# Kernel tuning notes

Hardware: AMD Instinct MI355X
Metric: run time of the kernel (lower is better)

The kernel has to match this reference:

```python
import jax, jax.numpy as jnp
import numpy as np

C, T, H = 256, 16, 8
D = C // H  # head dim = 32
SCALE = float((D * T) ** 0.5)


def setup_inputs() -> dict:
    key = jax.random.key(0)
    kx, kk, kq, kv = jax.random.split(key, 4)
    B, P = 8, 1024
    x = jax.random.normal(kx, (B, C, P, T), dtype=jnp.float32)
    # 1x1 conv weights, no bias -> [out_ch, in_ch]
    Wk = jax.random.normal(kk, (C, C), dtype=jnp.float32) * 0.02
    Wq = jax.random.normal(kq, (C, C), dtype=jnp.float32) * 0.02
    Wv = jax.random.normal(kv, (C, C), dtype=jnp.float32) * 0.02
    return {"x": x, "Wk": Wk, "Wq": Wq, "Wv": Wv}


def _proj_split(W, x):
    # 1x1 conv == channel matmul, then split heads: b (h d) p t -> b h d p t
    B, _, P, Tt = x.shape
    y = jnp.einsum('oc,bcpt->bopt', W, x)
    return y.reshape(B, H, D, P, Tt)


def reference(x, Wk, Wq, Wv):
    B, _, P, Tt = x.shape
    k = _proj_split(Wk, x)  # [B,H,D,P,T]
    q = _proj_split(Wq, x)
    v = _proj_split(Wv, x)
    # energy over spatial positions, contracting head-dim and time
    energy = jnp.einsum('bhdpt,bhdqt->bhpq', k, q)  # [B,H,P,P]
    attn = jax.nn.softmax(energy / SCALE, axis=-1)
    out = jnp.einsum('bhpq,bhdpt->bhdqt', attn, v)  # [B,H,D,P,T]
    return out.reshape(B, C, P, Tt)
```

## Files before the change

kernel.cpp:

```cpp
#include <hip/hip_runtime.h>


typedef unsigned short u16;
typedef unsigned int u32;
typedef __attribute__((ext_vector_type(8))) short bfx8;
typedef __attribute__((ext_vector_type(4))) float fx4;

constexpr float KC1 = 1.4426950408889634f / 22.627416997969522f;

__device__ __forceinline__ u16 f2bf(float f) {
  u32 u = __builtin_bit_cast(u32, f);
  return (u16)((u + 0x7fffu + ((u >> 16) & 1u)) >> 16);
}
__device__ __forceinline__ float bf2f(u16 v) {
  return __builtin_bit_cast(float, (u32)v << 16);
}
__device__ __forceinline__ fx4 mfma16(bfx8 a, bfx8 b, fx4 c) {
  return __builtin_amdgcn_mfma_f32_16x16x32_bf16(a, b, c, 0, 0, 0);
}
typedef __attribute__((address_space(1))) const unsigned int* as1p;
typedef __attribute__((address_space(3))) unsigned int* as3p;
__device__ __forceinline__ void gll16(const void* g, void* l) {
  __builtin_amdgcn_global_load_lds((as1p)g, (as3p)l, 16, 0, 0);
}

template <int NT, int LK>
__device__ __forceinline__ void gemm_core(const u16* __restrict__ Ag,
                                          const u16* __restrict__ Bg,
                                          u16 (&As)[3][16384], u16 (&Bs)[2][16384],
                                          fx4 (&acc)[8][4], int wv, int lane) {
  const int l15 = lane & 15, kg = lane >> 4, l7 = lane & 7;
  const int wq0 = (wv >> 2) * 128, wn0 = (wv & 3) * 64;
  const int rsub = lane >> 3, csub = (lane & 7) * 8;

  auto stageA = [&](int buf, int ks) {
#pragma unroll
    for (int i = 0; i < 4; ++i) {
      int r = wv * 32 + i * 8;
      gll16(Ag + (size_t)(r + rsub) * LK + ks * 64 + csub, &As[buf][r * 64]);
    }
  };
  auto stageB = [&](int buf, int ks) {
#pragma unroll
    for (int i = 0; i < 4; ++i) {
      int r = wv * 32 + i * 8;
      gll16(Bg + (size_t)(r + rsub) * LK + ks * 64 + csub, &Bs[buf][r * 64]);
    }
  };
  auto comp = [&](int ab, int bb) {
#pragma unroll
    for (int kk = 0; kk < 2; ++kk) {
      int csw = ((kk * 4 + kg) ^ l7) * 8;
      bfx8 af[8];
#pragma unroll
      for (int mt = 0; mt < 8; ++mt)
        af[mt] = *(const bfx8*)&As[ab][(wq0 + mt * 16 + l15) * 64 + csw];
#pragma unroll
      for (int nt = 0; nt < 4; ++nt) {
        bfx8 bf = *(const bfx8*)&Bs[bb][(wn0 + nt * 16 + l15) * 64 + csw];
#pragma unroll
        for (int mt = 0; mt < 8; ++mt) acc[mt][nt] = mfma16(af[mt], bf, acc[mt][nt]);
      }
    }
  };

  stageA(0, 0);
  stageB(0, 0);
  stageA(1, 1);
  stageB(1, 1);
  asm volatile("s_waitcnt vmcnt(8)" ::: "memory");
  __builtin_amdgcn_s_barrier();
  __builtin_amdgcn_sched_barrier(0);

  int ca = 0;
#pragma unroll 1
  for (int t = 0; t < NT; ++t) {
    const int cb = t & 1;
    if (t + 2 < NT) {
      int ca2 = ca + 2; if (ca2 >= 3) ca2 -= 3;
      stageA(ca2, t + 2);
    }
    __builtin_amdgcn_s_setprio(1);
    comp(ca, cb);
    __builtin_amdgcn_s_setprio(0);
    if (t + 1 < NT) {
      if (t + 2 < NT) {
        asm volatile("s_waitcnt vmcnt(4)" ::: "memory");
      } else {
        asm volatile("s_waitcnt vmcnt(0)" ::: "memory");
      }
      __builtin_amdgcn_s_barrier();
      __builtin_amdgcn_sched_barrier(0);
      if (t + 2 < NT) stageB(cb, t + 2);
    }
    ca = (ca == 2) ? 0 : ca + 1;
  }
}

__global__ __launch_bounds__(256) void k_wconv(const float* __restrict__ Wk,
                                               const float* __restrict__ Wq,
                                               const float* __restrict__ Wv,
                                               u16* __restrict__ Wall) {
  int blk = blockIdx.x;
  int pr = blk >> 5;
  const float* src = (pr == 0) ? Wk : ((pr == 1) ? Wq : Wv);
  int oc = (blk & 31) * 8 + (threadIdx.x >> 5);
  int Cc = threadIdx.x & 31;
  const float4* s4 = (const float4*)(src + oc * 256 + Cc * 8);
  float4 a = s4[0], b = s4[1];
  alignas(16) u16 t[8] = {f2bf(a.x), f2bf(a.y), f2bf(a.z), f2bf(a.w),
                          f2bf(b.x), f2bf(b.y), f2bf(b.z), f2bf(b.w)};
  int o = pr * 256 + oc;
  int pos = (Cc & ~7) + ((Cc & 7) ^ (o & 7));
  *(uint4*)(Wall + o * 256 + pos * 8) = *(const uint4*)t;
}

__global__ __launch_bounds__(256) void k_xt(const float* __restrict__ x,
                                            u16* __restrict__ Xbf) {
  __shared__ u16 Xs[128 * 256];
  int b = blockIdx.x >> 7;
  int n0 = (blockIdx.x & 127) * 128;
  int tid = threadIdx.x;
  int ng = tid & 31, cgrp = tid >> 5;
  const float* xb = x + (size_t)b * 4194304 + n0 + ng * 4;
#pragma unroll
  for (int it = 0; it < 4; ++it) {
    int Cc = cgrp + it * 8;
    float4 v[8];
#pragma unroll
    for (int i = 0; i < 8; ++i)
      v[i] = *(const float4*)(xb + (size_t)(Cc * 8 + i) * 16384);
#pragma unroll
    for (int j = 0; j < 4; ++j) {
      int n = ng * 4 + j;
      alignas(16) u16 c8[8];
#pragma unroll
      for (int i = 0; i < 8; ++i) c8[i] = f2bf(((const float*)&v[i])[j]);
      int pos = (Cc & ~7) + ((Cc & 7) ^ (n & 7));
      *(uint4*)&Xs[n * 256 + pos * 8] = *(const uint4*)c8;
    }
  }
  __syncthreads();
  u16* xo = Xbf + (size_t)b * 4194304 + (size_t)n0 * 256;
#pragma unroll
  for (int it = 0; it < 16; ++it) {
    int idx = tid + it * 256;
    int n = idx >> 5, chp = idx & 31;
    uint4 v = *(const uint4*)&Xs[n * 256 + chp * 8];
    *(uint4*)&xo[(size_t)n * 256 + chp * 8] = v;
  }
}

__global__ __launch_bounds__(512) void k_proj2(const u16* __restrict__ Xbf,
                                               const u16* __restrict__ Wall,
                                               u16* __restrict__ Kb, u16* __restrict__ Qb,
                                               u16* __restrict__ Vb) {
  __shared__ u16 As[3][16384];
  __shared__ u16 Bs[2][16384];
  int bid = blockIdx.x;
  int vid = (bid & 7) * 192 + (bid >> 3);
  int nidx = vid / 3;
  int otile = vid - nidx * 3;
  int b = nidx >> 6, ntile = nidx & 63;
  int tid = threadIdx.x, lane = tid & 63, wv = tid >> 6;
  int l15 = lane & 15, kg = lane >> 4;
  int wq0 = (wv >> 2) * 128;
  const u16* Ag = Wall + otile * 65536;
  const u16* Bg = Xbf + (size_t)b * 4194304 + (size_t)ntile * 65536;
  fx4 acc[8][4];
#pragma unroll
  for (int mt = 0; mt < 8; ++mt)
#pragma unroll
    for (int nt = 0; nt < 4; ++nt) acc[mt][nt] = (fx4)0.0f;

  gemm_core<4, 256>(Ag, Bg, As, Bs, acc, wv, lane);

  u16* dst = (otile == 0) ? Kb : ((otile == 1) ? Qb : Vb);
#pragma unroll
  for (int mt = 0; mt < 8; ++mt) {
    int oc = wq0 + mt * 16 + kg * 4;
    int h = oc >> 5;
    size_t bhro = (size_t)(b * 8 + h) * 524288;
#pragma unroll
    for (int nt = 0; nt < 4; ++nt) {
      int p = ntile * 16 + (wv & 3) * 4 + nt;
      size_t ro = bhro + (size_t)p * 512;
      int p7 = p & 7;
#pragma unroll
      for (int j = 0; j < 4; ++j) {
        int f = ((oc & 31) + j) * 16 + l15;
        int ch = (f >> 3) ^ p7;
        dst[ro + ch * 8 + (f & 7)] = f2bf(acc[mt][nt][j]);
      }
    }
  }
}

__global__ __launch_bounds__(512) void k_egemm(const u16* __restrict__ Qb,
                                               const u16* __restrict__ Kb,
                                               u16* __restrict__ Pt,
                                               float* __restrict__ Zpart) {
  __shared__ u16 As[3][16384];
  __shared__ u16 Bs[2][16384];
  int bid = blockIdx.x;
  int vid = (bid & 7) * 128 + (bid >> 3);
  int bh = vid >> 4, tile = vid & 15;
  int q0 = (tile >> 2) * 256, p0 = (tile & 3) * 256;
  int tid = threadIdx.x, lane = tid & 63, wv = tid >> 6;
  int l15 = lane & 15, kg = lane >> 4;
  int wq0 = (wv >> 2) * 128, wp0 = (wv & 3) * 64;
  const u16* Ag = Qb + (size_t)bh * 524288 + (size_t)q0 * 512;
  const u16* Bg = Kb + (size_t)bh * 524288 + (size_t)p0 * 512;
  fx4 acc[8][4];
#pragma unroll
  for (int mt = 0; mt < 8; ++mt)
#pragma unroll
    for (int nt = 0; nt < 4; ++nt) acc[mt][nt] = (fx4)0.0f;

  gemm_core<8, 512>(Ag, Bg, As, Bs, acc, wv, lane);

  float zl[4] = {0.f, 0.f, 0.f, 0.f};
  size_t pbase = (size_t)bh * 1048576;
#pragma unroll
  for (int mt = 0; mt < 8; ++mt) {
    int qb_ = q0 + wq0 + mt * 16 + kg * 4;
#pragma unroll
    for (int nt = 0; nt < 4; ++nt) {
      int p = p0 + wp0 + nt * 16 + l15;
#pragma unroll
      for (int j = 0; j < 4; ++j) {
        int q = qb_ + j;
        float e = exp2f(acc[mt][nt][j] * KC1);
        zl[nt] += e;
        Pt[pbase + (size_t)q * 1024 + (((p >> 3) ^ (q & 7)) * 8 + (p & 7))] = f2bf(e);
      }
    }
  }
  float* Zl = (float*)&As[0][0];
#pragma unroll
  for (int nt = 0; nt < 4; ++nt) {
    float v = zl[nt];
    v += __shfl_xor(v, 16);
    v += __shfl_xor(v, 32);
    zl[nt] = v;
  }
  if (lane < 16) {
#pragma unroll
    for (int nt = 0; nt < 4; ++nt)
      Zl[(wv >> 2) * 256 + wp0 + nt * 16 + lane] = zl[nt];
  }
  __syncthreads();
  if (tid < 256) {
    float s = Zl[tid] + Zl[256 + tid];
    Zpart[(size_t)(tile >> 2) * 65536 + (size_t)bh * 1024 + p0 + tid] = s;
  }
}

__global__ __launch_bounds__(256) void k_zfinal(const float* __restrict__ Zpart,
                                                float* __restrict__ RZ) {
  int idx = blockIdx.x * 256 + threadIdx.x;
  float s = Zpart[idx] + Zpart[65536 + idx] + Zpart[131072 + idx] + Zpart[196608 + idx];
  RZ[idx] = 1.0f / s;
}

__global__ __launch_bounds__(256) void k_vt(const u16* __restrict__ Vb,
                                            const float* __restrict__ RZ,
                                            u16* __restrict__ Vt) {
  __shared__ u16 Vl[64 * 512];
  int bh = blockIdx.x >> 4;
  int ptile = blockIdx.x & 15;
  int tid = threadIdx.x;
  const u16* src = Vb + (size_t)bh * 524288 + (size_t)ptile * 32768;
#pragma unroll
  for (int it = 0; it < 16; ++it) {
    int idx = tid + it * 256;
    int pl = idx >> 6, g = idx & 63;
    float rz = RZ[bh * 1024 + ptile * 64 + pl];
    uint4 v = *(const uint4*)&src[(size_t)pl * 512 + g * 8];
    int cf = g ^ (pl & 7);
    u32 w[4] = {v.x, v.y, v.z, v.w};
    alignas(16) u16 c8[8];
#pragma unroll
    for (int i = 0; i < 4; ++i) {
      c8[2 * i]     = f2bf(bf2f((u16)w[i]) * rz);
      c8[2 * i + 1] = f2bf(bf2f((u16)(w[i] >> 16)) * rz);
    }
    *(uint4*)&Vl[pl * 512 + cf * 8] = *(const uint4*)c8;
  }
  __syncthreads();
  u16* dst = Vt + (size_t)bh * 524288;
#pragma unroll
  for (int it = 0; it < 16; ++it) {
    int f = (tid & 63) + (it & 7) * 64;
    int pc = (tid >> 6) * 2 + (it >> 3);
    int base = pc * 8 * 512 + f;
    u32 x0 = (u32)Vl[base] | ((u32)Vl[base + 512] << 16);
    u32 x1 = (u32)Vl[base + 1024] | ((u32)Vl[base + 1536] << 16);
    u32 x2 = (u32)Vl[base + 2048] | ((u32)Vl[base + 2560] << 16);
    u32 x3 = (u32)Vl[base + 3072] | ((u32)Vl[base + 3584] << 16);
    uint4 pk; pk.x = x0; pk.y = x1; pk.z = x2; pk.w = x3;
    int col = ptile * 8 + (pc ^ (f & 7));
    *(uint4*)&dst[(size_t)f * 1024 + col * 8] = pk;
  }
}

__global__ __launch_bounds__(512) void k_pv(const u16* __restrict__ Pt,
                                            const u16* __restrict__ Vt,
                                            float* __restrict__ out) {
  __shared__ u16 As[3][16384];
  __shared__ u16 Bs[2][16384];
  int bid = blockIdx.x;
  int vid = (bid & 7) * 64 + (bid >> 3);
  int bh = vid >> 3, tile = vid & 7;
  int q0 = (tile >> 1) * 256, f0 = (tile & 1) * 256;
  int tid = threadIdx.x, lane = tid & 63, wv = tid >> 6;
  int l15 = lane & 15, kg = lane >> 4;
  int wq0 = (wv >> 2) * 128, wf0 = (wv & 3) * 64;
  const u16* Ag = Pt + (size_t)bh * 1048576 + (size_t)q0 * 1024;
  const u16* Bg = Vt + (size_t)bh * 524288 + (size_t)f0 * 1024;
  fx4 acc[8][4];
#pragma unroll
  for (int mt = 0; mt < 8; ++mt)
#pragma unroll
    for (int nt = 0; nt < 4; ++nt) acc[mt][nt] = (fx4)0.0f;

  gemm_core<16, 1024>(Ag, Bg, As, Bs, acc, wv, lane);

#pragma unroll
  for (int mt = 0; mt < 8; ++mt) {
    int qb_ = q0 + wq0 + mt * 16 + kg * 4;
#pragma unroll
    for (int nt = 0; nt < 4; ++nt) {
      int f = f0 + wf0 + nt * 16 + l15;
      int d = f >> 4, t = f & 15;
      size_t cb = (size_t)(bh * 32 + d) * 16384 + t;
#pragma unroll
      for (int j = 0; j < 4; ++j) out[cb + (size_t)(qb_ + j) * 16] = acc[mt][nt][j];
    }
  }
}

extern "C" void kernel_launch(void* const* d_in, const int* in_sizes, int n_in,
                              void* d_out, int out_size, void* d_ws, size_t ws_size,
                              hipStream_t stream) {
  (void)in_sizes; (void)n_in; (void)out_size; (void)ws_size;
  const float* x  = (const float*)d_in[0];
  const float* Wk = (const float*)d_in[1];
  const float* Wq = (const float*)d_in[2];
  const float* Wv = (const float*)d_in[3];
  float* out = (float*)d_out;

  u16* Kb  = (u16*)d_ws;
  u16* Qb  = Kb + 33554432;
  u16* Vb  = Qb + 33554432;
  u16* Xbf = Vb + 33554432;
  u16* Pt  = Xbf;
  u16* Vt  = Qb;
  float* Zpart = (float*)(Kb + 167772160);
  float* RZ = Zpart + 262144;
  u16* Wall = (u16*)(RZ + 65536);

  k_wconv<<<96, 256, 0, stream>>>(Wk, Wq, Wv, Wall);
  k_xt<<<1024, 256, 0, stream>>>(x, Xbf);
  k_proj2<<<1536, 512, 0, stream>>>(Xbf, Wall, Kb, Qb, Vb);
  k_egemm<<<1024, 512, 0, stream>>>(Qb, Kb, Pt, Zpart);
  k_zfinal<<<256, 256, 0, stream>>>(Zpart, RZ);
  k_vt<<<1024, 256, 0, stream>>>(Vb, RZ, Vt);
  k_pv<<<512, 512, 0, stream>>>(Pt, Vt, out);
}
```

Measured before the change: 389.0 us.

## Replace GEMM core with 8-phase ping-pong pipeline over half-tiles

Replaces the triple/double-buffered GEMM main loop shared by the projection, energy and PV kernels with an 8-phase schedule. It splits each 256x256 tile into M/N halves, double-buffers A and B in one LDS array, and interleaves half-tile global->LDS loads with register fragment loads and MFMA bursts between barriers. The warp-to-output mapping changes to 2x4 sub-blocks spread across halves, and the epilogues are adjusted to match. The aim is to overlap memory traffic with MFMA work at finer grain, at the cost of many more barriers per K step and tighter waitcnt bookkeeping.

```diff
diff --git a/kernel.cpp b/kernel.cpp
--- a/kernel.cpp
+++ b/kernel.cpp
@@ -23,77 +23,113 @@
 __device__ __forceinline__ void gll16(const void* g, void* l) {
   __builtin_amdgcn_global_load_lds((as1p)g, (as3p)l, 16, 0, 0);
 }
-
-template <int NT, int LK>
-__device__ __forceinline__ void gemm_core(const u16* __restrict__ Ag,
-                                          const u16* __restrict__ Bg,
-                                          u16 (&As)[3][16384], u16 (&Bs)[2][16384],
-                                          fx4 (&acc)[8][4], int wv, int lane) {
-  const int l15 = lane & 15, kg = lane >> 4, l7 = lane & 7;
-  const int wq0 = (wv >> 2) * 128, wn0 = (wv & 3) * 64;
-  const int rsub = lane >> 3, csub = (lane & 7) * 8;
-
-  auto stageA = [&](int buf, int ks) {
-#pragma unroll
-    for (int i = 0; i < 4; ++i) {
-      int r = wv * 32 + i * 8;
-      gll16(Ag + (size_t)(r + rsub) * LK + ks * 64 + csub, &As[buf][r * 64]);
-    }
-  };
-  auto stageB = [&](int buf, int ks) {
-#pragma unroll
-    for (int i = 0; i < 4; ++i) {
-      int r = wv * 32 + i * 8;
-      gll16(Bg + (size_t)(r + rsub) * LK + ks * 64 + csub, &Bs[buf][r * 64]);
-    }
-  };
-  auto comp = [&](int ab, int bb) {
-#pragma unroll
-    for (int kk = 0; kk < 2; ++kk) {
-      int csw = ((kk * 4 + kg) ^ l7) * 8;
-      bfx8 af[8];
-#pragma unroll
-      for (int mt = 0; mt < 8; ++mt)
-        af[mt] = *(const bfx8*)&As[ab][(wq0 + mt * 16 + l15) * 64 + csw];
-#pragma unroll
-      for (int nt = 0; nt < 4; ++nt) {
-        bfx8 bf = *(const bfx8*)&Bs[bb][(wn0 + nt * 16 + l15) * 64 + csw];
-#pragma unroll
-        for (int mt = 0; mt < 8; ++mt) acc[mt][nt] = mfma16(af[mt], bf, acc[mt][nt]);
-      }
-    }
-  };
-
-  stageA(0, 0);
-  stageB(0, 0);
-  stageA(1, 1);
-  stageB(1, 1);
-  asm volatile("s_waitcnt vmcnt(8)" ::: "memory");
+__device__ __forceinline__ void bar_() {
   __builtin_amdgcn_s_barrier();
   __builtin_amdgcn_sched_barrier(0);
-
-  int ca = 0;
+}
+__device__ __forceinline__ void lg0_() {
+  asm volatile("s_waitcnt lgkmcnt(0)" ::: "memory");
+  __builtin_amdgcn_sched_barrier(0);
+}
+#define VMC4 asm volatile("s_waitcnt vmcnt(4)" ::: "memory")
+#define VMC0 asm volatile("s_waitcnt vmcnt(0)" ::: "memory")
+
+template <int NT, int LK>
+__device__ __forceinline__ void gemm8(const u16* __restrict__ Ag,
+                                      const u16* __restrict__ Bg,
+                                      u16* lds, fx4 (&acc)[2][4][2][2],
+                                      int wv, int lane) {
+  const int l15 = lane & 15, kg = lane >> 4, l7 = lane & 7;
+  const int wr = wv >> 2, wn = wv & 3;
+  const int rsub = lane >> 3, csub = (lane & 7) * 8;
+  constexpr int A0 = 0, A1 = 16384, B0 = 32768, B1 = 49152;
+  bfx8 af[4][2], bf[2][2][2];
+
+  auto stg = [&](const u16* g, int ldsoff, int tile, int half) {
+    const u16* gp = g + (size_t)(half * 128 + wv * 16 + rsub) * LK + tile * 64 + csub;
+    u16* lp = lds + ldsoff + half * 8192 + wv * 1024;
+    gll16(gp, lp);
+    gll16(gp + (size_t)8 * LK, lp + 512);
+  };
+  auto LA = [&](int boff, int mh) {
+    const u16* base = lds + boff + mh * 8192 + wr * 4096;
+#pragma unroll
+    for (int mt = 0; mt < 4; ++mt)
+#pragma unroll
+      for (int kk = 0; kk < 2; ++kk)
+        af[mt][kk] = *(const bfx8*)(base + (mt * 16 + l15) * 64 + (((kk << 2) + kg) ^ l7) * 8);
+  };
+  auto LB = [&](int boff, int nh) {
+    const u16* base = lds + boff + nh * 8192 + wn * 2048;
+#pragma unroll
+    for (int nt = 0; nt < 2; ++nt)
+#pragma unroll
+      for (int kk = 0; kk < 2; ++kk)
+        bf[nh][nt][kk] = *(const bfx8*)(base + (nt * 16 + l15) * 64 + (((kk << 2) + kg) ^ l7) * 8);
+  };
+  auto MM = [&](int mh, int nh) {
+    __builtin_amdgcn_s_setprio(1);
+#pragma unroll
+    for (int mt = 0; mt < 4; ++mt)
+#pragma unroll
+      for (int nt = 0; nt < 2; ++nt)
+#pragma unroll
+        for (int kk = 0; kk < 2; ++kk)
+          acc[mh][mt][nh][nt] = mfma16(af[mt][kk], bf[nh][nt][kk], acc[mh][mt][nh][nt]);
+    __builtin_amdgcn_s_setprio(0);
+  };
+
+  stg(Ag, A0, 0, 0); stg(Ag, A0, 0, 1);
+  stg(Bg, B0, 0, 0); stg(Bg, B0, 0, 1);
+  stg(Ag, A1, 1, 0); stg(Bg, B1, 1, 1);
+  VMC4;
+  bar_();
+
+  constexpr int NI = NT / 2;
 #pragma unroll 1
-  for (int t = 0; t < NT; ++t) {
-    const int cb = t & 1;
-    if (t + 2 < NT) {
-      int ca2 = ca + 2; if (ca2 >= 3) ca2 -= 3;
-      stageA(ca2, t + 2);
-    }
-    __builtin_amdgcn_s_setprio(1);
-    comp(ca, cb);
-    __builtin_amdgcn_s_setprio(0);
-    if (t + 1 < NT) {
-      if (t + 2 < NT) {
-        asm volatile("s_waitcnt vmcnt(4)" ::: "memory");
-      } else {
-        asm volatile("s_waitcnt vmcnt(0)" ::: "memory");
-      }
-      __builtin_amdgcn_s_barrier();
-      __builtin_amdgcn_sched_barrier(0);
-      if (t + 2 < NT) stageB(cb, t + 2);
-    }
-    ca = (ca == 2) ? 0 : ca + 1;
+  for (int i = 0; i < NI; ++i) {
+    const int t = 2 * i;
+    const bool more = (i + 1 < NI);
+    LA(A0, 0); LB(B0, 0);
+    stg(Ag, A1, t + 1, 1);
+    bar_(); lg0_();
+    MM(0, 0);
+    bar_();
+    LB(B0, 1);
+    stg(Bg, B1, t + 1, 0);
+    bar_(); lg0_();
+    MM(0, 1);
+    bar_();
+    LA(A0, 1);
+    if (more) stg(Ag, A0, t + 2, 0);
+    bar_(); lg0_();
+    MM(1, 1);
+    bar_();
+    if (more) stg(Bg, B0, t + 2, 1);
+    bar_();
+    MM(1, 0);
+    if (more) { VMC4; } else { VMC0; }
+    bar_();
+    LA(A1, 0); LB(B1, 0);
+    if (more) stg(Ag, A0, t + 2, 1);
+    bar_(); lg0_();
+    MM(0, 0);
+    bar_();
+    LB(B1, 1);
+    if (more) stg(Bg, B0, t + 2, 0);
+    bar_(); lg0_();
+    MM(0, 1);
+    bar_();
+    LA(A1, 1);
+    if (more) stg(Ag, A1, t + 3, 0);
+    bar_(); lg0_();
+    MM(1, 1);
+    bar_();
+    if (more) stg(Bg, B1, t + 3, 1);
+    bar_();
+    MM(1, 0);
+    if (more) { VMC4; }
+    bar_();
   }
 }
 
@@ -155,8 +191,7 @@
                                                const u16* __restrict__ Wall,
                                                u16* __restrict__ Kb, u16* __restrict__ Qb,
                                                u16* __restrict__ Vb) {
-  __shared__ u16 As[3][16384];
-  __shared__ u16 Bs[2][16384];
+  __shared__ u16 lds[65536];
   int bid = blockIdx.x;
   int vid = (bid & 7) * 192 + (bid >> 3);
   int nidx = vid / 3;
@@ -164,90 +199,110 @@
   int b = nidx >> 6, ntile = nidx & 63;
   int tid = threadIdx.x, lane = tid & 63, wv = tid >> 6;
   int l15 = lane & 15, kg = lane >> 4;
-  int wq0 = (wv >> 2) * 128;
+  int wr = wv >> 2, wn = wv & 3;
   const u16* Ag = Wall + otile * 65536;
   const u16* Bg = Xbf + (size_t)b * 4194304 + (size_t)ntile * 65536;
-  fx4 acc[8][4];
-#pragma unroll
-  for (int mt = 0; mt < 8; ++mt)
-#pragma unroll
-    for (int nt = 0; nt < 4; ++nt) acc[mt][nt] = (fx4)0.0f;
-
-  gemm_core<4, 256>(Ag, Bg, As, Bs, acc, wv, lane);
+  fx4 acc[2][4][2][2];
+#pragma unroll
+  for (int mh = 0; mh < 2; ++mh)
+#pragma unroll
+    for (int mt = 0; mt < 4; ++mt)
+#pragma unroll
+      for (int nh = 0; nh < 2; ++nh)
+#pragma unroll
+        for (int nt = 0; nt < 2; ++nt) acc[mh][mt][nh][nt] = (fx4)0.0f;
+
+  gemm8<4, 256>(Ag, Bg, lds, acc, wv, lane);
 
   u16* dst = (otile == 0) ? Kb : ((otile == 1) ? Qb : Vb);
 #pragma unroll
-  for (int mt = 0; mt < 8; ++mt) {
-    int oc = wq0 + mt * 16 + kg * 4;
-    int h = oc >> 5;
-    size_t bhro = (size_t)(b * 8 + h) * 524288;
-#pragma unroll
-    for (int nt = 0; nt < 4; ++nt) {
-      int p = ntile * 16 + (wv & 3) * 4 + nt;
-      size_t ro = bhro + (size_t)p * 512;
-      int p7 = p & 7;
-#pragma unroll
-      for (int j = 0; j < 4; ++j) {
-        int f = ((oc & 31) + j) * 16 + l15;
-        int ch = (f >> 3) ^ p7;
-        dst[ro + ch * 8 + (f & 7)] = f2bf(acc[mt][nt][j]);
-      }
-    }
-  }
+  for (int mh = 0; mh < 2; ++mh)
+#pragma unroll
+    for (int mt = 0; mt < 4; ++mt) {
+      int o = mh * 128 + wr * 64 + mt * 16 + kg * 4;
+      int h = o >> 5;
+      size_t bhro = (size_t)(b * 8 + h) * 524288;
+#pragma unroll
+      for (int nh = 0; nh < 2; ++nh)
+#pragma unroll
+        for (int nt = 0; nt < 2; ++nt) {
+          int p = ntile * 16 + nh * 8 + wn * 2 + nt;
+          size_t ro = bhro + (size_t)p * 512;
+          int p7 = p & 7;
+#pragma unroll
+          for (int j = 0; j < 4; ++j) {
+            int f = ((o & 31) + j) * 16 + l15;
+            int ch = (f >> 3) ^ p7;
+            dst[ro + ch * 8 + (f & 7)] = f2bf(acc[mh][mt][nh][nt][j]);
+          }
+        }
+    }
 }
 
 __global__ __launch_bounds__(512) void k_egemm(const u16* __restrict__ Qb,
                                                const u16* __restrict__ Kb,
                                                u16* __restrict__ Pt,
                                                float* __restrict__ Zpart) {
-  __shared__ u16 As[3][16384];
-  __shared__ u16 Bs[2][16384];
+  __shared__ u16 lds[65536];
   int bid = blockIdx.x;
   int vid = (bid & 7) * 128 + (bid >> 3);
   int bh = vid >> 4, tile = vid & 15;
   int q0 = (tile >> 2) * 256, p0 = (tile & 3) * 256;
   int tid = threadIdx.x, lane = tid & 63, wv = tid >> 6;
   int l15 = lane & 15, kg = lane >> 4;
-  int wq0 = (wv >> 2) * 128, wp0 = (wv & 3) * 64;
+  int wr = wv >> 2, wn = wv & 3;
   const u16* Ag = Qb + (size_t)bh * 524288 + (size_t)q0 * 512;
   const u16* Bg = Kb + (size_t)bh * 524288 + (size_t)p0 * 512;
-  fx4 acc[8][4];
-#pragma unroll
-  for (int mt = 0; mt < 8; ++mt)
-#pragma unroll
-    for (int nt = 0; nt < 4; ++nt) acc[mt][nt] = (fx4)0.0f;
-
-  gemm_core<8, 512>(Ag, Bg, As, Bs, acc, wv, lane);
-
-  float zl[4] = {0.f, 0.f, 0.f, 0.f};
+  fx4 acc[2][4][2][2];
+#pragma unroll
+  for (int mh = 0; mh < 2; ++mh)
+#pragma unroll
+    for (int mt = 0; mt < 4; ++mt)
+#pragma unroll
+      for (int nh = 0; nh < 2; ++nh)
+#pragma unroll
+        for (int nt = 0; nt < 2; ++nt) acc[mh][mt][nh][nt] = (fx4)0.0f;
+
+  gemm8<8, 512>(Ag, Bg, lds, acc, wv, lane);
+
+  float zl[2][2] = {{0.f, 0.f}, {0.f, 0.f}};
   size_t pbase = (size_t)bh * 1048576;
 #pragma unroll
-  for (int mt = 0; mt < 8; ++mt) {
-    int qb_ = q0 + wq0 + mt * 16 + kg * 4;
-#pragma unroll
-    for (int nt = 0; nt < 4; ++nt) {
-      int p = p0 + wp0 + nt * 16 + l15;
-#pragma unroll
-      for (int j = 0; j < 4; ++j) {
-        int q = qb_ + j;
-        float e = exp2f(acc[mt][nt][j] * KC1);
-        zl[nt] += e;
-        Pt[pbase + (size_t)q * 1024 + (((p >> 3) ^ (q & 7)) * 8 + (p & 7))] = f2bf(e);
-      }
-    }
-  }
-  float* Zl = (float*)&As[0][0];
-#pragma unroll
-  for (int nt = 0; nt < 4; ++nt) {
-    float v = zl[nt];
-    v += __shfl_xor(v, 16);
-    v += __shfl_xor(v, 32);
-    zl[nt] = v;
-  }
+  for (int mh = 0; mh < 2; ++mh)
+#pragma unroll
+    for (int mt = 0; mt < 4; ++mt) {
+      int qb_ = q0 + mh * 128 + wr * 64 + mt * 16 + kg * 4;
+#pragma unroll
+      for (int nh = 0; nh < 2; ++nh)
+#pragma unroll
+        for (int nt = 0; nt < 2; ++nt) {
+          int p = p0 + nh * 128 + wn * 32 + nt * 16 + l15;
+#pragma unroll
+          for (int j = 0; j < 4; ++j) {
+            int q = qb_ + j;
+            float e = exp2f(acc[mh][mt][nh][nt][j] * KC1);
+            zl[nh][nt] += e;
+            Pt[pbase + (size_t)q * 1024 + (((p >> 3) ^ (q & 7)) * 8 + (p & 7))] = f2bf(e);
+          }
+        }
+    }
+  float* Zl = (float*)lds;
+#pragma unroll
+  for (int nh = 0; nh < 2; ++nh)
+#pragma unroll
+    for (int nt = 0; nt < 2; ++nt) {
+      float v = zl[nh][nt];
+      v += __shfl_xor(v, 16);
+      v += __shfl_xor(v, 32);
+      zl[nh][nt] = v;
+    }
+  __syncthreads();
   if (lane < 16) {
 #pragma unroll
-    for (int nt = 0; nt < 4; ++nt)
-      Zl[(wv >> 2) * 256 + wp0 + nt * 16 + lane] = zl[nt];
+    for (int nh = 0; nh < 2; ++nh)
+#pragma unroll
+      for (int nt = 0; nt < 2; ++nt)
+        Zl[wr * 256 + nh * 128 + wn * 32 + nt * 16 + lane] = zl[nh][nt];
   }
   __syncthreads();
   if (tid < 256) {
@@ -307,37 +362,44 @@
 __global__ __launch_bounds__(512) void k_pv(const u16* __restrict__ Pt,
                                             const u16* __restrict__ Vt,
                                             float* __restrict__ out) {
-  __shared__ u16 As[3][16384];
-  __shared__ u16 Bs[2][16384];
+  __shared__ u16 lds[65536];
   int bid = blockIdx.x;
   int vid = (bid & 7) * 64 + (bid >> 3);
   int bh = vid >> 3, tile = vid & 7;
   int q0 = (tile >> 1) * 256, f0 = (tile & 1) * 256;
   int tid = threadIdx.x, lane = tid & 63, wv = tid >> 6;
   int l15 = lane & 15, kg = lane >> 4;
-  int wq0 = (wv >> 2) * 128, wf0 = (wv & 3) * 64;
+  int wr = wv >> 2, wn = wv & 3;
   const u16* Ag = Pt + (size_t)bh * 1048576 + (size_t)q0 * 1024;
   const u16* Bg = Vt + (size_t)bh * 524288 + (size_t)f0 * 1024;
-  fx4 acc[8][4];
-#pragma unroll
-  for (int mt = 0; mt < 8; ++mt)
-#pragma unroll
-    for (int nt = 0; nt < 4; ++nt) acc[mt][nt] = (fx4)0.0f;
-
-  gemm_core<16, 1024>(Ag, Bg, As, Bs, acc, wv, lane);
-
-#pragma unroll
-  for (int mt = 0; mt < 8; ++mt) {
-    int qb_ = q0 + wq0 + mt * 16 + kg * 4;
-#pragma unroll
-    for (int nt = 0; nt < 4; ++nt) {
-      int f = f0 + wf0 + nt * 16 + l15;
-      int d = f >> 4, t = f & 15;
-      size_t cb = (size_t)(bh * 32 + d) * 16384 + t;
-#pragma unroll
-      for (int j = 0; j < 4; ++j) out[cb + (size_t)(qb_ + j) * 16] = acc[mt][nt][j];
-    }
-  }
+  fx4 acc[2][4][2][2];
+#pragma unroll
+  for (int mh = 0; mh < 2; ++mh)
+#pragma unroll
+    for (int mt = 0; mt < 4; ++mt)
+#pragma unroll
+      for (int nh = 0; nh < 2; ++nh)
+#pragma unroll
+        for (int nt = 0; nt < 2; ++nt) acc[mh][mt][nh][nt] = (fx4)0.0f;
+
+  gemm8<16, 1024>(Ag, Bg, lds, acc, wv, lane);
+
+#pragma unroll
+  for (int mh = 0; mh < 2; ++mh)
+#pragma unroll
+    for (int mt = 0; mt < 4; ++mt) {
+      int qb_ = q0 + mh * 128 + wr * 64 + mt * 16 + kg * 4;
+#pragma unroll
+      for (int nh = 0; nh < 2; ++nh)
+#pragma unroll
+        for (int nt = 0; nt < 2; ++nt) {
+          int f = f0 + nh * 128 + wn * 32 + nt * 16 + l15;
+          int d = f >> 4, t = f & 15;
+          size_t cb = (size_t)(bh * 32 + d) * 16384 + t;
+#pragma unroll
+          for (int j = 0; j < 4; ++j) out[cb + (size_t)(qb_ + j) * 16] = acc[mh][mt][nh][nt][j];
+        }
+    }
 }
 
 extern "C" void kernel_launch(void* const* d_in, const int* in_sizes, int n_in,
```

Measured after the change: 352.7 us. 9.3% less time.

## Replace pipelined 256x256 GEMM core with simple 128x128 single-buffer tiles

Applied to the files above, without the earlier changes.

Swaps the triple/double-buffered 256x256 GEMM core (512 threads, about 160KB of LDS) for a simpler 128x128 tile using 256 threads and 32KB of LDS with launch_bounds occupancy 3. This trades data reuse and explicit load/compute overlap for higher occupancy, so several blocks per CU can hide latency. The energy GEMM swaps its MFMA operands so each lane can write 4 contiguous bf16 P values as one 64-bit store, and the Z partial sums grow to 16 slices with shuffle reductions. Risks include more global/L2 traffic from smaller tiles and the loss of the software pipeline, since there is a sync before and after every load stage.

```diff
diff --git a/kernel.cpp b/kernel.cpp
--- a/kernel.cpp
+++ b/kernel.cpp
@@ -3,6 +3,7 @@
 
 typedef unsigned short u16;
 typedef unsigned int u32;
+typedef unsigned long long u64;
 typedef __attribute__((ext_vector_type(8))) short bfx8;
 typedef __attribute__((ext_vector_type(4))) float fx4;
 
@@ -24,76 +25,49 @@
   __builtin_amdgcn_global_load_lds((as1p)g, (as3p)l, 16, 0, 0);
 }
 
-template <int NT, int LK>
-__device__ __forceinline__ void gemm_core(const u16* __restrict__ Ag,
-                                          const u16* __restrict__ Bg,
-                                          u16 (&As)[3][16384], u16 (&Bs)[2][16384],
-                                          fx4 (&acc)[8][4], int wv, int lane) {
+template <bool SWAP, int NT, int LK>
+__device__ __forceinline__ void gemm97(const u16* __restrict__ Ag,
+                                       const u16* __restrict__ Bg,
+                                       u16* lds, fx4 (&acc)[4][4],
+                                       int wv, int lane) {
   const int l15 = lane & 15, kg = lane >> 4, l7 = lane & 7;
-  const int wq0 = (wv >> 2) * 128, wn0 = (wv & 3) * 64;
+  const int wr = wv >> 1, wc = wv & 1;
   const int rsub = lane >> 3, csub = (lane & 7) * 8;
-
-  auto stageA = [&](int buf, int ks) {
+  bfx8 af[4][2], bf[4][2];
+
+#pragma unroll 1
+  for (int t = 0; t < NT; ++t) {
+    __syncthreads();
 #pragma unroll
     for (int i = 0; i < 4; ++i) {
       int r = wv * 32 + i * 8;
-      gll16(Ag + (size_t)(r + rsub) * LK + ks * 64 + csub, &As[buf][r * 64]);
-    }
-  };
-  auto stageB = [&](int buf, int ks) {
-#pragma unroll
-    for (int i = 0; i < 4; ++i) {
-      int r = wv * 32 + i * 8;
-      gll16(Bg + (size_t)(r + rsub) * LK + ks * 64 + csub, &Bs[buf][r * 64]);
-    }
-  };
-  auto comp = [&](int ab, int bb) {
-#pragma unroll
-    for (int kk = 0; kk < 2; ++kk) {
-      int csw = ((kk * 4 + kg) ^ l7) * 8;
-      bfx8 af[8];
-#pragma unroll
-      for (int mt = 0; mt < 8; ++mt)
-        af[mt] = *(const bfx8*)&As[ab][(wq0 + mt * 16 + l15) * 64 + csw];
-#pragma unroll
-      for (int nt = 0; nt < 4; ++nt) {
-        bfx8 bf = *(const bfx8*)&Bs[bb][(wn0 + nt * 16 + l15) * 64 + csw];
-#pragma unroll
-        for (int mt = 0; mt < 8; ++mt) acc[mt][nt] = mfma16(af[mt], bf, acc[mt][nt]);
-      }
-    }
-  };
-
-  stageA(0, 0);
-  stageB(0, 0);
-  stageA(1, 1);
-  stageB(1, 1);
-  asm volatile("s_waitcnt vmcnt(8)" ::: "memory");
-  __builtin_amdgcn_s_barrier();
-  __builtin_amdgcn_sched_barrier(0);
-
-  int ca = 0;
-#pragma unroll 1
-  for (int t = 0; t < NT; ++t) {
-    const int cb = t & 1;
-    if (t + 2 < NT) {
-      int ca2 = ca + 2; if (ca2 >= 3) ca2 -= 3;
-      stageA(ca2, t + 2);
-    }
-    __builtin_amdgcn_s_setprio(1);
-    comp(ca, cb);
-    __builtin_amdgcn_s_setprio(0);
-    if (t + 1 < NT) {
-      if (t + 2 < NT) {
-        asm volatile("s_waitcnt vmcnt(4)" ::: "memory");
-      } else {
-        asm volatile("s_waitcnt vmcnt(0)" ::: "memory");
-      }
-      __builtin_amdgcn_s_barrier();
-      __builtin_amdgcn_sched_barrier(0);
-      if (t + 2 < NT) stageB(cb, t + 2);
-    }
-    ca = (ca == 2) ? 0 : ca + 1;
+      gll16(Ag + (size_t)(r + rsub) * LK + t * 64 + csub, lds + r * 64);
+      gll16(Bg + (size_t)(r + rsub) * LK + t * 64 + csub, lds + 8192 + r * 64);
+    }
+    __syncthreads();
+#pragma unroll
+    for (int mt = 0; mt < 4; ++mt)
+#pragma unroll
+      for (int kk = 0; kk < 2; ++kk)
+        af[mt][kk] = *(const bfx8*)(lds + (wr * 64 + mt * 16 + l15) * 64 +
+                                    (((kk << 2) + kg) ^ l7) * 8);
+#pragma unroll
+    for (int nt = 0; nt < 4; ++nt)
+#pragma unroll
+      for (int kk = 0; kk < 2; ++kk)
+        bf[nt][kk] = *(const bfx8*)(lds + 8192 + (wc * 64 + nt * 16 + l15) * 64 +
+                                    (((kk << 2) + kg) ^ l7) * 8);
+#pragma unroll
+    for (int mt = 0; mt < 4; ++mt)
+#pragma unroll
+      for (int nt = 0; nt < 4; ++nt)
+#pragma unroll
+        for (int kk = 0; kk < 2; ++kk) {
+          if constexpr (SWAP)
+            acc[mt][nt] = mfma16(bf[nt][kk], af[mt][kk], acc[mt][nt]);
+          else
+            acc[mt][nt] = mfma16(af[mt][kk], bf[nt][kk], acc[mt][nt]);
+        }
   }
 }
 
@@ -133,11 +107,11 @@
 #pragma unroll
     for (int j = 0; j < 4; ++j) {
       int n = ng * 4 + j;
-      alignas(16) u16 c8[8];
-#pragma unroll
-      for (int i = 0; i < 8; ++i) c8[i] = f2bf(((const float*)&v[i])[j]);
+      alignas(16) u16 c8v[8];
+#pragma unroll
+      for (int i = 0; i < 8; ++i) c8v[i] = f2bf(((const float*)&v[i])[j]);
       int pos = (Cc & ~7) + ((Cc & 7) ^ (n & 7));
-      *(uint4*)&Xs[n * 256 + pos * 8] = *(const uint4*)c8;
+      *(uint4*)&Xs[n * 256 + pos * 8] = *(const uint4*)c8v;
     }
   }
   __syncthreads();
@@ -151,44 +125,46 @@
   }
 }
 
-__global__ __launch_bounds__(512) void k_proj2(const u16* __restrict__ Xbf,
-                                               const u16* __restrict__ Wall,
-                                               u16* __restrict__ Kb, u16* __restrict__ Qb,
-                                               u16* __restrict__ Vb) {
-  __shared__ u16 As[3][16384];
-  __shared__ u16 Bs[2][16384];
+__global__ __launch_bounds__(256, 3) void k_proj2(const u16* __restrict__ Xbf,
+                                                  const u16* __restrict__ Wall,
+                                                  u16* __restrict__ Kb, u16* __restrict__ Qb,
+                                                  u16* __restrict__ Vb) {
+  __shared__ u16 lds[16384];
   int bid = blockIdx.x;
-  int vid = (bid & 7) * 192 + (bid >> 3);
-  int nidx = vid / 3;
-  int otile = vid - nidx * 3;
-  int b = nidx >> 6, ntile = nidx & 63;
+  int vid = (bid & 7) * 768 + (bid >> 3);
+  int b = vid / 768;
+  int rem = vid - b * 768;
+  int mtile = rem >> 7, ntile = rem & 127;
   int tid = threadIdx.x, lane = tid & 63, wv = tid >> 6;
   int l15 = lane & 15, kg = lane >> 4;
-  int wq0 = (wv >> 2) * 128;
-  const u16* Ag = Wall + otile * 65536;
-  const u16* Bg = Xbf + (size_t)b * 4194304 + (size_t)ntile * 65536;
-  fx4 acc[8][4];
-#pragma unroll
-  for (int mt = 0; mt < 8; ++mt)
+  int wr = wv >> 1, wc = wv & 1;
+  const u16* Ag = Wall + mtile * 32768;
+  const u16* Bg = Xbf + (size_t)b * 4194304 + (size_t)ntile * 32768;
+  fx4 acc[4][4];
+#pragma unroll
+  for (int mt = 0; mt < 4; ++mt)
 #pragma unroll
     for (int nt = 0; nt < 4; ++nt) acc[mt][nt] = (fx4)0.0f;
 
-  gemm_core<4, 256>(Ag, Bg, As, Bs, acc, wv, lane);
-
-  u16* dst = (otile == 0) ? Kb : ((otile == 1) ? Qb : Vb);
-#pragma unroll
-  for (int mt = 0; mt < 8; ++mt) {
-    int oc = wq0 + mt * 16 + kg * 4;
+  gemm97<false, 4, 256>(Ag, Bg, lds, acc, wv, lane);
+
+  int pr = mtile >> 1;
+  u16* dst = (pr == 0) ? Kb : ((pr == 1) ? Qb : Vb);
+  int obase = (mtile & 1) * 128 + wr * 64;
+#pragma unroll
+  for (int mt = 0; mt < 4; ++mt) {
+    int oc = obase + mt * 16 + kg * 4;
     int h = oc >> 5;
     size_t bhro = (size_t)(b * 8 + h) * 524288;
 #pragma unroll
     for (int nt = 0; nt < 4; ++nt) {
-      int p = ntile * 16 + (wv & 3) * 4 + nt;
+      int n = ntile * 128 + wc * 64 + nt * 16 + l15;
+      int p = n >> 4, tt = n & 15;
       size_t ro = bhro + (size_t)p * 512;
       int p7 = p & 7;
 #pragma unroll
       for (int j = 0; j < 4; ++j) {
-        int f = ((oc & 31) + j) * 16 + l15;
+        int f = ((oc & 31) + j) * 16 + tt;
         int ch = (f >> 3) ^ p7;
         dst[ro + ch * 8 + (f & 7)] = f2bf(acc[mt][nt][j]);
       }
@@ -196,70 +172,85 @@
   }
 }
 
-__global__ __launch_bounds__(512) void k_egemm(const u16* __restrict__ Qb,
-                                               const u16* __restrict__ Kb,
-                                               u16* __restrict__ Pt,
-                                               float* __restrict__ Zpart) {
-  __shared__ u16 As[3][16384];
-  __shared__ u16 Bs[2][16384];
+__global__ __launch_bounds__(256, 3) void k_egemm(const u16* __restrict__ Qb,
+                                                  const u16* __restrict__ Kb,
+                                                  u16* __restrict__ Pt,
+                                                  float* __restrict__ Zpart) {
+  __shared__ u16 lds[16384];
   int bid = blockIdx.x;
-  int vid = (bid & 7) * 128 + (bid >> 3);
-  int bh = vid >> 4, tile = vid & 15;
-  int q0 = (tile >> 2) * 256, p0 = (tile & 3) * 256;
+  int vid = (bid & 7) * 512 + (bid >> 3);
+  int bh = vid >> 6;
+  int rem = vid & 63;
+  int qt = rem >> 3, pt = rem & 7;
+  int q0 = qt * 128, p0 = pt * 128;
   int tid = threadIdx.x, lane = tid & 63, wv = tid >> 6;
   int l15 = lane & 15, kg = lane >> 4;
-  int wq0 = (wv >> 2) * 128, wp0 = (wv & 3) * 64;
+  int wr = wv >> 1, wc = wv & 1;
   const u16* Ag = Qb + (size_t)bh * 524288 + (size_t)q0 * 512;
   const u16* Bg = Kb + (size_t)bh * 524288 + (size_t)p0 * 512;
-  fx4 acc[8][4];
-#pragma unroll
-  for (int mt = 0; mt < 8; ++mt)
+  fx4 acc[4][4];
+#pragma unroll
+  for (int mt = 0; mt < 4; ++mt)
 #pragma unroll
     for (int nt = 0; nt < 4; ++nt) acc[mt][nt] = (fx4)0.0f;
 
-  gemm_core<8, 512>(Ag, Bg, As, Bs, acc, wv, lane);
-
-  float zl[4] = {0.f, 0.f, 0.f, 0.f};
+  gemm97<true, 8, 512>(Ag, Bg, lds, acc, wv, lane);
+
   size_t pbase = (size_t)bh * 1048576;
-#pragma unroll
-  for (int mt = 0; mt < 8; ++mt) {
-    int qb_ = q0 + wq0 + mt * 16 + kg * 4;
+  float zac[4][4];
+#pragma unroll
+  for (int nt = 0; nt < 4; ++nt)
+#pragma unroll
+    for (int j = 0; j < 4; ++j) zac[nt][j] = 0.f;
+#pragma unroll
+  for (int mt = 0; mt < 4; ++mt) {
+    int q = q0 + wr * 64 + mt * 16 + l15;
+    size_t qrow = pbase + (size_t)q * 1024;
+    int q7 = l15 & 7;
 #pragma unroll
     for (int nt = 0; nt < 4; ++nt) {
-      int p = p0 + wp0 + nt * 16 + l15;
+      int p4 = p0 + wc * 64 + nt * 16 + kg * 4;
+      alignas(8) u16 e4[4];
 #pragma unroll
       for (int j = 0; j < 4; ++j) {
-        int q = qb_ + j;
         float e = exp2f(acc[mt][nt][j] * KC1);
-        zl[nt] += e;
-        Pt[pbase + (size_t)q * 1024 + (((p >> 3) ^ (q & 7)) * 8 + (p & 7))] = f2bf(e);
+        zac[nt][j] += e;
+        e4[j] = f2bf(e);
       }
-    }
-  }
-  float* Zl = (float*)&As[0][0];
-#pragma unroll
-  for (int nt = 0; nt < 4; ++nt) {
-    float v = zl[nt];
-    v += __shfl_xor(v, 16);
-    v += __shfl_xor(v, 32);
-    zl[nt] = v;
-  }
-  if (lane < 16) {
-#pragma unroll
-    for (int nt = 0; nt < 4; ++nt)
-      Zl[(wv >> 2) * 256 + wp0 + nt * 16 + lane] = zl[nt];
-  }
-  __syncthreads();
-  if (tid < 256) {
-    float s = Zl[tid] + Zl[256 + tid];
-    Zpart[(size_t)(tile >> 2) * 65536 + (size_t)bh * 1024 + p0 + tid] = s;
+      int ch = (p4 >> 3) ^ q7;
+      *(u64*)(Pt + qrow + ch * 8 + (p4 & 7)) = *(const u64*)e4;
+    }
+  }
+#pragma unroll
+  for (int nt = 0; nt < 4; ++nt)
+#pragma unroll
+    for (int j = 0; j < 4; ++j) {
+      float v = zac[nt][j];
+      v += __shfl_xor(v, 1);
+      v += __shfl_xor(v, 2);
+      v += __shfl_xor(v, 4);
+      v += __shfl_xor(v, 8);
+      zac[nt][j] = v;
+    }
+  if (l15 == 0) {
+    size_t zb = (size_t)(qt * 2 + wr) * 65536 + (size_t)bh * 1024;
+#pragma unroll
+    for (int nt = 0; nt < 4; ++nt) {
+      int p4 = p0 + wc * 64 + nt * 16 + kg * 4;
+      float4 zv;
+      zv.x = zac[nt][0]; zv.y = zac[nt][1];
+      zv.z = zac[nt][2]; zv.w = zac[nt][3];
+      *(float4*)&Zpart[zb + p4] = zv;
+    }
   }
 }
 
 __global__ __launch_bounds__(256) void k_zfinal(const float* __restrict__ Zpart,
                                                 float* __restrict__ RZ) {
   int idx = blockIdx.x * 256 + threadIdx.x;
-  float s = Zpart[idx] + Zpart[65536 + idx] + Zpart[131072 + idx] + Zpart[196608 + idx];
+  float s = 0.f;
+#pragma unroll
+  for (int k = 0; k < 16; ++k) s += Zpart[(size_t)k * 65536 + idx];
   RZ[idx] = 1.0f / s;
 }
 
@@ -279,13 +270,13 @@
     uint4 v = *(const uint4*)&src[(size_t)pl * 512 + g * 8];
     int cf = g ^ (pl & 7);
     u32 w[4] = {v.x, v.y, v.z, v.w};
-    alignas(16) u16 c8[8];
+    alignas(16) u16 c8v[8];
 #pragma unroll
     for (int i = 0; i < 4; ++i) {
-      c8[2 * i]     = f2bf(bf2f((u16)w[i]) * rz);
-      c8[2 * i + 1] = f2bf(bf2f((u16)(w[i] >> 16)) * rz);
-    }
-    *(uint4*)&Vl[pl * 512 + cf * 8] = *(const uint4*)c8;
+      c8v[2 * i]     = f2bf(bf2f((u16)w[i]) * rz);
+      c8v[2 * i + 1] = f2bf(bf2f((u16)(w[i] >> 16)) * rz);
+    }
+    *(uint4*)&Vl[pl * 512 + cf * 8] = *(const uint4*)c8v;
   }
   __syncthreads();
   u16* dst = Vt + (size_t)bh * 524288;
@@ -304,38 +295,40 @@
   }
 }
 
-__global__ __launch_bounds__(512) void k_pv(const u16* __restrict__ Pt,
-                                            const u16* __restrict__ Vt,
-                                            float* __restrict__ out) {
-  __shared__ u16 As[3][16384];
-  __shared__ u16 Bs[2][16384];
+__global__ __launch_bounds__(256, 3) void k_pv(const u16* __restrict__ Pt,
+                                               const u16* __restrict__ Vt,
+                                               float* __restrict__ out) {
+  __shared__ u16 lds[16384];
   int bid = blockIdx.x;
-  int vid = (bid & 7) * 64 + (bid >> 3);
-  int bh = vid >> 3, tile = vid & 7;
-  int q0 = (tile >> 1) * 256, f0 = (tile & 1) * 256;
+  int vid = (bid & 7) * 256 + (bid >> 3);
+  int bh = vid >> 5;
+  int rem = vid & 31;
+  int qt = rem >> 2, ft = rem & 3;
+  int q0 = qt * 128, f0 = ft * 128;
   int tid = threadIdx.x, lane = tid & 63, wv = tid >> 6;
   int l15 = lane & 15, kg = lane >> 4;
-  int wq0 = (wv >> 2) * 128, wf0 = (wv & 3) * 64;
+  int wr = wv >> 1, wc = wv & 1;
   const u16* Ag = Pt + (size_t)bh * 1048576 + (size_t)q0 * 1024;
   const u16* Bg = Vt + (size_t)bh * 524288 + (size_t)f0 * 1024;
-  fx4 acc[8][4];
-#pragma unroll
-  for (int mt = 0; mt < 8; ++mt)
+  fx4 acc[4][4];
+#pragma unroll
+  for (int mt = 0; mt < 4; ++mt)
 #pragma unroll
     for (int nt = 0; nt < 4; ++nt) acc[mt][nt] = (fx4)0.0f;
 
-  gemm_core<16, 1024>(Ag, Bg, As, Bs, acc, wv, lane);
-
-#pragma unroll
-  for (int mt = 0; mt < 8; ++mt) {
-    int qb_ = q0 + wq0 + mt * 16 + kg * 4;
+  gemm97<false, 16, 1024>(Ag, Bg, lds, acc, wv, lane);
+
+#pragma unroll
+  for (int mt = 0; mt < 4; ++mt) {
+    int qb_ = q0 + wr * 64 + mt * 16 + kg * 4;
 #pragma unroll
     for (int nt = 0; nt < 4; ++nt) {
-      int f = f0 + wf0 + nt * 16 + l15;
+      int f = f0 + wc * 64 + nt * 16 + l15;
       int d = f >> 4, t = f & 15;
       size_t cb = (size_t)(bh * 32 + d) * 16384 + t;
 #pragma unroll
-      for (int j = 0; j < 4; ++j) out[cb + (size_t)(qb_ + j) * 16] = acc[mt][nt][j];
+      for (int j = 0; j < 4; ++j)
+        out[cb + (size_t)(qb_ + j) * 16] = acc[mt][nt][j];
     }
   }
 }
@@ -357,14 +350,14 @@
   u16* Pt  = Xbf;
   u16* Vt  = Qb;
   float* Zpart = (float*)(Kb + 167772160);
-  float* RZ = Zpart + 262144;
+  float* RZ = Zpart + 1048576;
   u16* Wall = (u16*)(RZ + 65536);
 
   k_wconv<<<96, 256, 0, stream>>>(Wk, Wq, Wv, Wall);
   k_xt<<<1024, 256, 0, stream>>>(x, Xbf);
-  k_proj2<<<1536, 512, 0, stream>>>(Xbf, Wall, Kb, Qb, Vb);
-  k_egemm<<<1024, 512, 0, stream>>>(Qb, Kb, Pt, Zpart);
+  k_proj2<<<6144, 256, 0, stream>>>(Xbf, Wall, Kb, Qb, Vb);
+  k_egemm<<<4096, 256, 0, stream>>>(Qb, Kb, Pt, Zpart);
   k_zfinal<<<256, 256, 0, stream>>>(Zpart, RZ);
   k_vt<<<1024, 256, 0, stream>>>(Vb, RZ, Vt);
-  k_pv<<<512, 512, 0, stream>>>(Pt, Vt, out);
-}
+  k_pv<<<2048, 256, 0, stream>>>(Pt, Vt, out);
+}
```

Result: no change. 395.1 us (+1.6%).
